# Performance work log

Measured on AMD Instinct MI355X. Metric: run time of the kernel, lower is better.

## Reference

```python
import jax, jax.numpy as jnp
import numpy as np

N_NODES = 100000   # adj is [N, N], x is [N, D]
N_EDGES = 625000   # nnz of the COO adjacency
D_FEAT = 128       # embedding dim
EDGE_DROPOUT = 0.1


def setup_inputs() -> dict:
    key = jax.random.key(0)
    k1, k2, k3, k4 = jax.random.split(key, 4)
    x = jax.random.normal(k1, (N_NODES, D_FEAT), dtype=jnp.float32)
    edge_vals = jax.random.uniform(k2, (N_EDGES,), dtype=jnp.float32)
    edge_index = jax.random.randint(k3, (2, N_EDGES), 0, N_NODES)
    # training-mode edge dropout mask: keep edge iff u > edge_dropout
    keep_mask = jax.random.uniform(k4, (N_EDGES,)) > EDGE_DROPOUT
    return {"x": x, "edge_vals": edge_vals, "edge_index": edge_index, "keep_mask": keep_mask}


def reference(x, edge_vals, edge_index, keep_mask):
    # Dropping an edge from the COO tensor == zeroing its value in the SpMM.
    vals = jnp.where(keep_mask, edge_vals, jnp.zeros((), dtype=edge_vals.dtype))
    row = edge_index[0]  # destination rows of adj
    col = edge_index[1]  # source columns of adj
    # out[r] = sum_{e: row[e]==r} vals[e] * x[col[e]]   (torch.sparse.mm(adj, x))
    msgs = vals[:, None] * x[col]                      # [E, D]
    return jax.ops.segment_sum(msgs, row, num_segments=N_NODES)
```

## Files before the change

kernel.cpp:

```cpp
#include <hip/hip_runtime.h>

#define N_NODES 100000
#define N_EDGES 625000
#define D_FEAT  128

#define BKT_SHIFT 10
#define BKT_ROWS  1024
#define NBKT      ((N_NODES + BKT_ROWS - 1) / BKT_ROWS)
#define EPB       4096
#define ABLOCKS   ((N_EDGES + EPB - 1) / EPB)
#define CHCAP     80
#define CAPB      8192
#define CONV_BLOCKS (N_NODES * D_FEAT / 8 / 256)

#define BF_LO(u) __uint_as_float((u) << 16)
#define BF_HI(u) __uint_as_float((u) & 0xffff0000u)

__device__ __forceinline__ unsigned int rne_bf16(unsigned int u) {
    return (u + 0x7fffu + ((u >> 16) & 1u)) >> 16;
}

__global__ __launch_bounds__(256) void bucket_conv(
    const float* __restrict__ x, uint4* __restrict__ xb4,
    const int* __restrict__ ei, const int* __restrict__ keep,
    const float* __restrict__ vals,
    int*  __restrict__ counts,
    int2* __restrict__ chunks)
{
    int b = blockIdx.x;
    if (b < ABLOCKS) {
        __shared__ int cur[NBKT];
        int t = threadIdx.x;
        if (t < NBKT) cur[t] = 0;
        __syncthreads();
        int base = b * EPB;
        #pragma unroll
        for (int j = 0; j < 16; ++j) {
            int e = base + j * 256 + t;
            if (e < N_EDGES && keep[e]) {
                int r = ei[e];
                int bk = r >> BKT_SHIFT;
                int pos = atomicAdd(&cur[bk], 1);
                if (pos < CHCAP) {
                    int2 pr = { ei[N_EDGES + e] | ((r & (BKT_ROWS - 1)) << 17),
                                __float_as_int(vals[e]) };
                    chunks[((long long)b * NBKT + bk) * CHCAP + pos] = pr;
                }
            }
        }
        __syncthreads();
        if (t < NBKT) counts[b * NBKT + t] = min(cur[t], CHCAP);
    } else {
        int i = (b - ABLOCKS) * 256 + threadIdx.x;
        const float4* x4 = reinterpret_cast<const float4*>(x);
        float4 v0 = x4[i * 2], v1 = x4[i * 2 + 1];
        unsigned int a  = rne_bf16(__float_as_uint(v0.x));
        unsigned int bb = rne_bf16(__float_as_uint(v0.y));
        unsigned int c  = rne_bf16(__float_as_uint(v0.z));
        unsigned int d  = rne_bf16(__float_as_uint(v0.w));
        unsigned int e2 = rne_bf16(__float_as_uint(v1.x));
        unsigned int f  = rne_bf16(__float_as_uint(v1.y));
        unsigned int g  = rne_bf16(__float_as_uint(v1.z));
        unsigned int h  = rne_bf16(__float_as_uint(v1.w));
        uint4 o = { a | (bb << 16), c | (d << 16), e2 | (f << 16), g | (h << 16) };
        xb4[i] = o;
    }
}

__global__ __launch_bounds__(256) void build_csr(
    const int* __restrict__ counts, const int2* __restrict__ chunks,
    int2* __restrict__ fin, int2* __restrict__ rowinfo)
{
    __shared__ int2 ebuf[CAPB];
    __shared__ int  cbase[ABLOCKS + 1];
    __shared__ int  hist[BKT_ROWS];
    __shared__ int  ssum[256];
    int b = blockIdx.x, t = threadIdx.x;

    int c0 = (t < ABLOCKS) ? counts[t * NBKT + b] : 0;
    ssum[t] = c0;
    __syncthreads();
    for (int off = 1; off < 256; off <<= 1) {
        int add = (t >= off) ? ssum[t - off] : 0;
        __syncthreads();
        ssum[t] += add;
        __syncthreads();
    }
    int excl = (t == 0) ? 0 : ssum[t - 1];
    if (t < ABLOCKS) cbase[t] = excl;
    if (t == 255) cbase[ABLOCKS] = ssum[255];
    __syncthreads();
    int ntot = cbase[ABLOCKS]; if (ntot > CAPB) ntot = CAPB;

    if (t < ABLOCKS) {
        int n  = counts[t * NBKT + b];
        int cb = cbase[t];
        const int2* src = chunks + ((long long)t * NBKT + b) * CHCAP;
        for (int k = 0; k < n; ++k) {
            int dst = cb + k;
            if (dst < CAPB) ebuf[dst] = src[k];
        }
    }
    for (int i = t; i < BKT_ROWS; i += 256) hist[i] = 0;
    __syncthreads();

    for (int i = t; i < ntot; i += 256)
        atomicAdd(&hist[(ebuf[i].x >> 17) & (BKT_ROWS - 1)], 1);
    __syncthreads();

    int t4 = t * 4;
    int h0 = hist[t4], h1 = hist[t4 + 1], h2 = hist[t4 + 2], h3 = hist[t4 + 3];
    ssum[t] = h0 + h1 + h2 + h3;
    __syncthreads();
    for (int off = 1; off < 256; off <<= 1) {
        int add = (t >= off) ? ssum[t - off] : 0;
        __syncthreads();
        ssum[t] += add;
        __syncthreads();
    }
    int ex = (t == 0) ? 0 : ssum[t - 1];
    int s0 = ex, s1 = ex + h0, s2 = ex + h0 + h1, s3 = ex + h0 + h1 + h2;
    hist[t4] = s0; hist[t4 + 1] = s1; hist[t4 + 2] = s2; hist[t4 + 3] = s3;

    int rbase = b << BKT_SHIFT;
    int gbase = b * CAPB;
    int st[4] = { s0, s1, s2, s3 };
    int hh[4] = { h0, h1, h2, h3 };
    #pragma unroll
    for (int i = 0; i < 4; ++i) {
        int row = rbase + t4 + i;
        if (row < N_NODES) {
            int2 ri = { gbase + st[i], hh[i] };
            rowinfo[row] = ri;
        }
    }
    __syncthreads();

    for (int i = t; i < ntot; i += 256) {
        int2 pr = ebuf[i];
        int rl = (pr.x >> 17) & (BKT_ROWS - 1);
        int pos = atomicAdd(&hist[rl], 1);
        if (pos < CAPB) {
            int2 o = { pr.x & 0x1FFFF, pr.y };
            fin[gbase + pos] = o;
        }
    }
}

__global__ __launch_bounds__(256) void gather_csr_bf16(
    const uint4* __restrict__ xb4, const int2* __restrict__ rowinfo,
    const int2* __restrict__ fin, float4* __restrict__ out4)
{
    int gid = blockIdx.x * blockDim.x + threadIdx.x;
    int wave = gid >> 6;
    int lane = threadIdx.x & 63;
    int sub = lane >> 4, l16 = lane & 15;
    int row = wave * 4 + sub;
    if (row >= N_NODES) return;
    int2 ri = rowinfo[row];
    const int2* bp = fin + ri.x;
    int n = ri.y;

    float a0=0,a1=0,a2=0,a3=0,a4=0,a5=0,a6=0,a7=0;
    float c0=0,c1=0,c2=0,c3=0,c4=0,c5=0,c6=0,c7=0;
    int p = 0;
    if (p + 2 <= n) {
        int2 d0 = bp[0], d1 = bp[1];
        for (; p + 4 <= n; p += 2) {
            int2 nd0 = bp[p + 2], nd1 = bp[p + 3];
            uint4 g0 = xb4[(long long)d0.x * 16 + l16];
            uint4 g1 = xb4[(long long)d1.x * 16 + l16];
            float v0 = __int_as_float(d0.y), v1 = __int_as_float(d1.y);
            a0 += v0 * BF_LO(g0.x); a1 += v0 * BF_HI(g0.x);
            a2 += v0 * BF_LO(g0.y); a3 += v0 * BF_HI(g0.y);
            a4 += v0 * BF_LO(g0.z); a5 += v0 * BF_HI(g0.z);
            a6 += v0 * BF_LO(g0.w); a7 += v0 * BF_HI(g0.w);
            c0 += v1 * BF_LO(g1.x); c1 += v1 * BF_HI(g1.x);
            c2 += v1 * BF_LO(g1.y); c3 += v1 * BF_HI(g1.y);
            c4 += v1 * BF_LO(g1.z); c5 += v1 * BF_HI(g1.z);
            c6 += v1 * BF_LO(g1.w); c7 += v1 * BF_HI(g1.w);
            d0 = nd0; d1 = nd1;
        }
        {
            uint4 g0 = xb4[(long long)d0.x * 16 + l16];
            uint4 g1 = xb4[(long long)d1.x * 16 + l16];
            float v0 = __int_as_float(d0.y), v1 = __int_as_float(d1.y);
            a0 += v0 * BF_LO(g0.x); a1 += v0 * BF_HI(g0.x);
            a2 += v0 * BF_LO(g0.y); a3 += v0 * BF_HI(g0.y);
            a4 += v0 * BF_LO(g0.z); a5 += v0 * BF_HI(g0.z);
            a6 += v0 * BF_LO(g0.w); a7 += v0 * BF_HI(g0.w);
            c0 += v1 * BF_LO(g1.x); c1 += v1 * BF_HI(g1.x);
            c2 += v1 * BF_LO(g1.y); c3 += v1 * BF_HI(g1.y);
            c4 += v1 * BF_LO(g1.z); c5 += v1 * BF_HI(g1.z);
            c6 += v1 * BF_LO(g1.w); c7 += v1 * BF_HI(g1.w);
            p += 2;
        }
    }
    if (p < n) {
        int2 e = bp[p];
        uint4 g = xb4[(long long)e.x * 16 + l16];
        float v = __int_as_float(e.y);
        a0 += v * BF_LO(g.x); a1 += v * BF_HI(g.x);
        a2 += v * BF_LO(g.y); a3 += v * BF_HI(g.y);
        a4 += v * BF_LO(g.z); a5 += v * BF_HI(g.z);
        a6 += v * BF_LO(g.w); a7 += v * BF_HI(g.w);
    }
    float4 o0 = { a0 + c0, a1 + c1, a2 + c2, a3 + c3 };
    float4 o1 = { a4 + c4, a5 + c5, a6 + c6, a7 + c7 };
    long long ob = (long long)row * 32 + l16 * 2;
    out4[ob]     = o0;
    out4[ob + 1] = o1;
}

__global__ __launch_bounds__(256) void gather_csr_f32(
    const float* __restrict__ x, const int2* __restrict__ rowinfo,
    const int2* __restrict__ fin, float* __restrict__ out)
{
    int gid = blockIdx.x * blockDim.x + threadIdx.x;
    int row = gid >> 6;
    if (row >= N_NODES) return;
    int lane = threadIdx.x & 63;
    int2 ri = rowinfo[row];
    const int2* bp = fin + ri.x;
    int n = ri.y;
    int d = lane * 2;
    float a0 = 0.f, b0 = 0.f, a1 = 0.f, b1 = 0.f;
    int p = 0;
    for (; p + 2 <= n; p += 2) {
        int2 e0 = bp[p], e1 = bp[p + 1];
        float2 x0 = *reinterpret_cast<const float2*>(x + (long long)e0.x * D_FEAT + d);
        float2 x1 = *reinterpret_cast<const float2*>(x + (long long)e1.x * D_FEAT + d);
        float v0 = __int_as_float(e0.y), v1 = __int_as_float(e1.y);
        a0 += v0 * x0.x; b0 += v0 * x0.y;
        a1 += v1 * x1.x; b1 += v1 * x1.y;
    }
    if (p < n) {
        int2 e = bp[p];
        float2 xv = *reinterpret_cast<const float2*>(x + (long long)e.x * D_FEAT + d);
        float v = __int_as_float(e.y);
        a0 += v * xv.x; b0 += v * xv.y;
    }
    float2 o = { a0 + a1, b0 + b1 };
    *reinterpret_cast<float2*>(out + (long long)row * D_FEAT + d) = o;
}

static inline size_t alignup(size_t v) { return (v + 511) / 512 * 512; }

extern "C" void kernel_launch(void* const* d_in, const int* in_sizes, int n_in,
                              void* d_out, int out_size, void* d_ws, size_t ws_size,
                              hipStream_t stream) {
    const float* x    = (const float*)d_in[0];
    const float* vals = (const float*)d_in[1];
    const int*   ei   = (const int*)d_in[2];
    const int*   keep = (const int*)d_in[3];
    float* out = (float*)d_out;

    const size_t sz_xb     = alignup((size_t)N_NODES * D_FEAT * 2);
    const size_t sz_counts = alignup((size_t)ABLOCKS * NBKT * 4);
    const size_t sz_chunks = alignup((size_t)ABLOCKS * NBKT * CHCAP * 8);
    const size_t sz_fin    = alignup((size_t)NBKT * CAPB * 8);
    const size_t sz_ri     = alignup((size_t)N_NODES * 8);
    const bool use_bf16 =
        ws_size >= sz_xb + sz_counts + sz_chunks + sz_fin + sz_ri;

    char* ws = (char*)d_ws;
    uint4* xb4 = nullptr;
    if (use_bf16) { xb4 = (uint4*)ws; ws += sz_xb; }
    int*  counts  = (int*)ws;   ws += sz_counts;
    int2* chunks  = (int2*)ws;  ws += sz_chunks;
    int2* fin     = (int2*)ws;  ws += sz_fin;
    int2* rowinfo = (int2*)ws;

    const int ablocks_total = use_bf16 ? (ABLOCKS + CONV_BLOCKS) : ABLOCKS;
    bucket_conv<<<ablocks_total, 256, 0, stream>>>(
        x, xb4, ei, keep, vals, counts, chunks);
    build_csr<<<NBKT, 256, 0, stream>>>(counts, chunks, fin, rowinfo);

    if (use_bf16) {
        const long long gthreads = (long long)((N_NODES + 3) / 4) * 64;
        gather_csr_bf16<<<(int)((gthreads + 255) / 256), 256, 0, stream>>>(
            xb4, rowinfo, fin, (float4*)out);
    } else {
        const long long gthreads = (long long)N_NODES * 64;
        gather_csr_f32<<<(int)((gthreads + 255) / 256), 256, 0, stream>>>(
            x, rowinfo, fin, out);
    }
}
```

Baseline: 75.57 us.

## Halve edges per bucketing block and batch edge loads before shared atomics

Each bucketing block now handles half as many edges, so twice as many blocks run and per-block chunk capacity is cut to match. The edge loads (keep mask, row, column, value) are issued together into registers before the shared-memory atomic loop, so memory latency is overlapped. The CSR builder scans two block counts per thread and copies chunks in a strided loop, because the block count now exceeds the thread count. The smaller per-chunk capacity raises the risk of silently dropping edges if a bucket overflows.

Result: faster. 69.68 us (-7.8%).

```diff
diff --git a/kernel.cpp b/kernel.cpp
--- a/kernel.cpp
+++ b/kernel.cpp
@@ -7,9 +7,9 @@
 #define BKT_SHIFT 10
 #define BKT_ROWS  1024
 #define NBKT      ((N_NODES + BKT_ROWS - 1) / BKT_ROWS)
-#define EPB       4096
+#define EPB       2048
 #define ABLOCKS   ((N_EDGES + EPB - 1) / EPB)
-#define CHCAP     80
+#define CHCAP     48
 #define CAPB      8192
 #define CONV_BLOCKS (N_NODES * D_FEAT / 8 / 256)
 
@@ -34,16 +34,24 @@
         if (t < NBKT) cur[t] = 0;
         __syncthreads();
         int base = b * EPB;
+        int kp[8], rows[8], cols[8]; float vv[8];
         #pragma unroll
-        for (int j = 0; j < 16; ++j) {
+        for (int j = 0; j < 8; ++j) {
             int e = base + j * 256 + t;
-            if (e < N_EDGES && keep[e]) {
-                int r = ei[e];
-                int bk = r >> BKT_SHIFT;
+            bool in = (e < N_EDGES);
+            kp[j]   = in ? keep[e] : 0;
+            rows[j] = in ? ei[e] : 0;
+            cols[j] = in ? ei[N_EDGES + e] : 0;
+            vv[j]   = in ? vals[e] : 0.f;
+        }
+        #pragma unroll
+        for (int j = 0; j < 8; ++j) {
+            if (kp[j]) {
+                int bk = rows[j] >> BKT_SHIFT;
                 int pos = atomicAdd(&cur[bk], 1);
                 if (pos < CHCAP) {
-                    int2 pr = { ei[N_EDGES + e] | ((r & (BKT_ROWS - 1)) << 17),
-                                __float_as_int(vals[e]) };
+                    int2 pr = { cols[j] | ((rows[j] & (BKT_ROWS - 1)) << 17),
+                                __float_as_int(vv[j]) };
                     chunks[((long long)b * NBKT + bk) * CHCAP + pos] = pr;
                 }
             }
@@ -77,8 +85,10 @@
     __shared__ int  ssum[256];
     int b = blockIdx.x, t = threadIdx.x;
 
-    int c0 = (t < ABLOCKS) ? counts[t * NBKT + b] : 0;
-    ssum[t] = c0;
+    int i0 = 2 * t, i1 = 2 * t + 1;
+    int c0 = (i0 < ABLOCKS) ? counts[i0 * NBKT + b] : 0;
+    int c1 = (i1 < ABLOCKS) ? counts[i1 * NBKT + b] : 0;
+    ssum[t] = c0 + c1;
     __syncthreads();
     for (int off = 1; off < 256; off <<= 1) {
         int add = (t >= off) ? ssum[t - off] : 0;
@@ -87,15 +97,16 @@
         __syncthreads();
     }
     int excl = (t == 0) ? 0 : ssum[t - 1];
-    if (t < ABLOCKS) cbase[t] = excl;
+    if (i0 < ABLOCKS) cbase[i0] = excl;
+    if (i1 < ABLOCKS) cbase[i1] = excl + c0;
     if (t == 255) cbase[ABLOCKS] = ssum[255];
     __syncthreads();
     int ntot = cbase[ABLOCKS]; if (ntot > CAPB) ntot = CAPB;
 
-    if (t < ABLOCKS) {
-        int n  = counts[t * NBKT + b];
-        int cb = cbase[t];
-        const int2* src = chunks + ((long long)t * NBKT + b) * CHCAP;
+    for (int c = t; c < ABLOCKS; c += 256) {
+        int n  = counts[c * NBKT + b];
+        int cb = cbase[c];
+        const int2* src = chunks + ((long long)c * NBKT + b) * CHCAP;
         for (int k = 0; k < n; ++k) {
             int dst = cb + k;
             if (dst < CAPB) ebuf[dst] = src[k];
```
